# Optimization experiments

Hardware: AMD Instinct MI355X
Metric: run time of the kernel (lower is better)

## Reference

```python
import jax, jax.numpy as jnp
import numpy as np

N_NODES = 4096  # nodes per graph (output1 reshaped to [-1, N_NODES])


def setup_inputs() -> dict:
    key = jax.random.key(0)
    ks = jax.random.split(key, 10)
    total_nodes = 64 * N_NODES          # 64 graphs of 4096 nodes
    n_edges = total_nodes * 8           # avg degree 8 lattice-like graph
    n_hidden = 128
    return {
        "node_features": jax.random.normal(ks[0], (total_nodes, 1), jnp.float32),
        "src": jax.random.randint(ks[1], (n_edges,), 0, total_nodes, jnp.int32),
        "dst": jax.random.randint(ks[2], (n_edges,), 0, total_nodes, jnp.int32),
        "w_self1": jax.random.normal(ks[3], (1, n_hidden), jnp.float32) * 0.5,
        "w_neigh1": jax.random.normal(ks[4], (1, n_hidden), jnp.float32) * 0.5,
        "b1": jnp.zeros((n_hidden,), jnp.float32),
        "w_self2": jax.random.normal(ks[5], (n_hidden, 1), jnp.float32) * (1.0 / np.sqrt(n_hidden)),
        "w_neigh2": jax.random.normal(ks[6], (n_hidden, 1), jnp.float32) * (1.0 / np.sqrt(n_hidden)),
        "b2": jnp.zeros((1,), jnp.float32),
        "w3": jax.random.normal(ks[7], (N_NODES, N_NODES), jnp.float32) * (1.0 / np.sqrt(N_NODES)),
        "b3": jnp.zeros((N_NODES,), jnp.float32),
    }


def _sage_mean(feat, src, dst, w_self, w_neigh, b, num_nodes):
    # gather source-node features along edges, mean-reduce at destination
    agg = jax.ops.segment_sum(feat[src], dst, num_segments=num_nodes)
    deg = jax.ops.segment_sum(jnp.ones((src.shape[0], 1), feat.dtype), dst,
                              num_segments=num_nodes)
    h_neigh = agg / jnp.maximum(deg, 1.0)
    return feat @ w_self + h_neigh @ w_neigh + b


def reference(node_features, src, dst, w_self1, w_neigh1, b1,
              w_self2, w_neigh2, b2, w3, b3):
    n = node_features.shape[0]
    h1 = jnp.tanh(_sage_mean(node_features, src, dst, w_self1, w_neigh1, b1, n))
    out1 = _sage_mean(h1, src, dst, w_self2, w_neigh2, b2, n)
    output1 = out1.reshape(-1, N_NODES)          # [batch, n_nodes]
    h2 = jnp.tanh(output1)
    output2 = h2 @ w3 + b3
    return (output1, output2)
```

## Files before the change

### kernel.cpp

```cpp
#include <hip/hip_runtime.h>


#define NTOT (64 * 4096)
#define NHID 128
#define GK   4096
#define KCH  256
#define KCHUNKS 16
#define GKC  128
#define GKCN 32
#define NBINS 128
#define BSZ   2048
#define BSH   11
#define CAP   17408
#define NSL   4
#define SCB   256

typedef unsigned int u32;

__device__ __forceinline__ float fast_tanh(float x) {
    float ax = fabsf(x);
    float t  = __expf(-2.0f * ax);
    float r  = (1.0f - t) / (1.0f + t);
    return copysignf(r, x);
}


__global__ void __launch_bounds__(1024) scatter_x(const int* __restrict__ src,
                                                  const int* __restrict__ dst,
                                                  int n_edges,
                                                  int* __restrict__ edge_cnt,
                                                  u32* __restrict__ packed) {
    __shared__ int lc[NBINS];
    __shared__ int lbase[NBINS];
    int t = threadIdx.x;
    if (t < NBINS) lc[t] = 0;
    __syncthreads();
    int per = (n_edges + gridDim.x - 1) / gridDim.x;
    int e0 = blockIdx.x * per;
    int e1 = min(e0 + per, n_edges);

    int dreg[8], sreg[8];
#pragma unroll
    for (int i = 0; i < 8; ++i) {
        int e = e0 + t + i * 1024;
        bool ok = e < e1;
        int d = ok ? dst[e] : -1;
        dreg[i] = d;
        sreg[i] = ok ? src[e] : 0;
        if (ok) atomicAdd(&lc[d >> BSH], 1);
    }
    __syncthreads();
    if (t < NBINS) {
        lbase[t] = atomicAdd(&edge_cnt[t], lc[t]);
        lc[t] = 0;
    }
    __syncthreads();
#pragma unroll
    for (int i = 0; i < 8; ++i) {
        int d = dreg[i];
        if (d >= 0) {
            int b = d >> BSH;
            int pos = lbase[b] + atomicAdd(&lc[b], 1);
            if (pos < CAP)
                packed[(size_t)b * CAP + pos] =
                    ((u32)(d & (BSZ - 1)) << 18) | (u32)sreg[i];
        }
    }
}

__global__ void __launch_bounds__(1024) agg1_x(const u32* __restrict__ packed,
                                               const int* __restrict__ edge_cnt,
                                               const float* __restrict__ nf,
                                               float* __restrict__ part1) {
    __shared__ float lsum[BSZ];
    __shared__ float lcnt[BSZ];
    int t = threadIdx.x;
    int b = blockIdx.x, s = blockIdx.y;
    for (int i = t; i < BSZ; i += 1024) { lsum[i] = 0.0f; lcnt[i] = 0.0f; }
    __syncthreads();
    int en  = min(edge_cnt[b], CAP);
    int per = (en + NSL - 1) / NSL;
    int e0  = s * per;
    int e1  = min(e0 + per, en);
    const u32* pk = packed + (size_t)b * CAP;
    for (int e = e0 + t; e < e1; e += 1024) {
        u32 p = pk[e];
        int local = (int)(p >> 18);
        atomicAdd(&lsum[local], nf[p & 0x3FFFFu]);
        atomicAdd(&lcnt[local], 1.0f);
    }
    __syncthreads();
    float* dp = part1 + ((size_t)(b * NSL + s) * 2) * BSZ;
    for (int i = t; i < BSZ; i += 1024) { dp[i] = lsum[i]; dp[BSZ + i] = lcnt[i]; }
}

__global__ void node1_x(const float* __restrict__ nf, const float* __restrict__ part1,
                        const float* __restrict__ w_s1, const float* __restrict__ w_n1,
                        const float* __restrict__ bb1,
                        const float* __restrict__ w_s2, const float* __restrict__ w_n2,
                        float* __restrict__ degf, float* __restrict__ selfp,
                        float* __restrict__ sp) {
    __shared__ float lws1[NHID], lwn1[NHID], lb1[NHID], lws2[NHID], lwn2[NHID];
    int tid = threadIdx.x;
    if (tid < NHID) {
        lws1[tid] = w_s1[tid];
        lwn1[tid] = w_n1[tid];
        lb1[tid]  = bb1[tid];
        lws2[tid] = w_s2[tid];
        lwn2[tid] = w_n2[tid];
    }
    __syncthreads();
    int v = blockIdx.x * blockDim.x + tid;
    int b = v >> BSH, local = v & (BSZ - 1);
    float sum = 0.0f, cf = 0.0f;
#pragma unroll
    for (int s = 0; s < NSL; ++s) {
        const float* dp = part1 + ((size_t)(b * NSL + s) * 2) * BSZ;
        sum += dp[local];
        cf  += dp[BSZ + local];
    }
    float hn = sum / fmaxf(cf, 1.0f);
    float f = nf[v];
    float a = 0.0f, s2 = 0.0f;
#pragma unroll 8
    for (int j = 0; j < NHID; ++j) {
        float t = fast_tanh(fmaf(f, lws1[j], fmaf(hn, lwn1[j], lb1[j])));
        a  = fmaf(t, lws2[j], a);
        s2 = fmaf(t, lwn2[j], s2);
    }
    degf[v]  = cf;
    selfp[v] = a;
    sp[v]    = s2;
}

__global__ void __launch_bounds__(1024) agg2_x(const u32* __restrict__ packed,
                                               const int* __restrict__ edge_cnt,
                                               const float* __restrict__ spv,
                                               float* __restrict__ part2) {
    __shared__ float lsum[BSZ];
    int t = threadIdx.x;
    int b = blockIdx.x, s = blockIdx.y;
    for (int i = t; i < BSZ; i += 1024) lsum[i] = 0.0f;
    __syncthreads();
    int en  = min(edge_cnt[b], CAP);
    int per = (en + NSL - 1) / NSL;
    int e0  = s * per;
    int e1  = min(e0 + per, en);
    const u32* pk = packed + (size_t)b * CAP;
    for (int e = e0 + t; e < e1; e += 1024) {
        u32 p = pk[e];
        atomicAdd(&lsum[p >> 18], spv[p & 0x3FFFFu]);
    }
    __syncthreads();
    float* dp = part2 + (size_t)(b * NSL + s) * BSZ;
    for (int i = t; i < BSZ; i += 1024) dp[i] = lsum[i];
}

__global__ void node2_x(const float* __restrict__ selfp, const float* __restrict__ part2,
                        const float* __restrict__ degf, const float* __restrict__ b2p,
                        const float* __restrict__ b3p,
                        float* __restrict__ out1, float* __restrict__ h2t,
                        float* __restrict__ out2) {
    int v = blockIdx.x * blockDim.x + threadIdx.x;
    int b = v >> BSH, local = v & (BSZ - 1);
    float agg2 = 0.0f;
#pragma unroll
    for (int s = 0; s < NSL; ++s)
        agg2 += part2[(size_t)(b * NSL + s) * BSZ + local];
    float o = selfp[v] + agg2 / fmaxf(degf[v], 1.0f) + b2p[0];
    out1[v] = o;
    int r = v >> 12;
    int k = v & 4095;
    h2t[k * 64 + r] = fast_tanh(o);
    out2[v] = b3p[v & 4095];
}

__global__ void __launch_bounds__(512, 4) gemm_x(const float* __restrict__ h2t,
                                                 const float* __restrict__ w3,
                                                 float* __restrict__ out2) {
    __shared__ float As[GKC * 64 + 64];
    int t    = threadIdx.x;
    int lane = t & 63;
    int wv   = t >> 6;
    int colb = blockIdx.x * 128 + lane * 2;
    int k0   = blockIdx.y * GKC;
    int row0 = __builtin_amdgcn_readfirstlane(wv * 8);

    const float4* gA = (const float4*)(h2t + (size_t)k0 * 64);
    float4* sA = (float4*)As;
#pragma unroll
    for (int i = 0; i < 4; ++i) sA[t + i * 512] = gA[t + i * 512];

    const float* wp  = w3 + (size_t)k0 * GK + colb;
    const float* Asw = As + row0;

    float2 acc[8];
#pragma unroll
    for (int r = 0; r < 8; ++r) { acc[r].x = 0.0f; acc[r].y = 0.0f; }

    float2 bvA[8], bvB[8];
#pragma unroll
    for (int j = 0; j < 8; ++j) bvA[j] = *(const float2*)(wp + (size_t)j * GK);

    __syncthreads();

    float4 a0 = *(const float4*)(Asw);
    float4 a1 = *(const float4*)(Asw + 4);

    for (int kk = 0; kk < GKC; kk += 16) {
#pragma unroll
        for (int j = 0; j < 8; ++j)
            bvB[j] = *(const float2*)(wp + (size_t)(kk + 8 + j) * GK);
#pragma unroll
        for (int j = 0; j < 8; ++j) {
            const float* An = Asw + (kk + j + 1) * 64;
            float4 n0 = *(const float4*)(An);
            float4 n1 = *(const float4*)(An + 4);
            float2 b  = bvA[j];
            acc[0].x = fmaf(a0.x, b.x, acc[0].x); acc[0].y = fmaf(a0.x, b.y, acc[0].y);
            acc[1].x = fmaf(a0.y, b.x, acc[1].x); acc[1].y = fmaf(a0.y, b.y, acc[1].y);
            acc[2].x = fmaf(a0.z, b.x, acc[2].x); acc[2].y = fmaf(a0.z, b.y, acc[2].y);
            acc[3].x = fmaf(a0.w, b.x, acc[3].x); acc[3].y = fmaf(a0.w, b.y, acc[3].y);
            acc[4].x = fmaf(a1.x, b.x, acc[4].x); acc[4].y = fmaf(a1.x, b.y, acc[4].y);
            acc[5].x = fmaf(a1.y, b.x, acc[5].x); acc[5].y = fmaf(a1.y, b.y, acc[5].y);
            acc[6].x = fmaf(a1.z, b.x, acc[6].x); acc[6].y = fmaf(a1.z, b.y, acc[6].y);
            acc[7].x = fmaf(a1.w, b.x, acc[7].x); acc[7].y = fmaf(a1.w, b.y, acc[7].y);
            a0 = n0; a1 = n1;
        }
        if (kk + 16 < GKC) {
#pragma unroll
            for (int j = 0; j < 8; ++j)
                bvA[j] = *(const float2*)(wp + (size_t)(kk + 16 + j) * GK);
        }
#pragma unroll
        for (int j = 0; j < 8; ++j) {
            const float* An = Asw + (kk + 8 + j + 1) * 64;
            float4 n0 = *(const float4*)(An);
            float4 n1 = *(const float4*)(An + 4);
            float2 b  = bvB[j];
            acc[0].x = fmaf(a0.x, b.x, acc[0].x); acc[0].y = fmaf(a0.x, b.y, acc[0].y);
            acc[1].x = fmaf(a0.y, b.x, acc[1].x); acc[1].y = fmaf(a0.y, b.y, acc[1].y);
            acc[2].x = fmaf(a0.z, b.x, acc[2].x); acc[2].y = fmaf(a0.z, b.y, acc[2].y);
            acc[3].x = fmaf(a0.w, b.x, acc[3].x); acc[3].y = fmaf(a0.w, b.y, acc[3].y);
            acc[4].x = fmaf(a1.x, b.x, acc[4].x); acc[4].y = fmaf(a1.x, b.y, acc[4].y);
            acc[5].x = fmaf(a1.y, b.x, acc[5].x); acc[5].y = fmaf(a1.y, b.y, acc[5].y);
            acc[6].x = fmaf(a1.z, b.x, acc[6].x); acc[6].y = fmaf(a1.z, b.y, acc[6].y);
            acc[7].x = fmaf(a1.w, b.x, acc[7].x); acc[7].y = fmaf(a1.w, b.y, acc[7].y);
            a0 = n0; a1 = n1;
        }
    }

    float* Cp = out2 + (size_t)row0 * GK + colb;
#pragma unroll
    for (int r = 0; r < 8; ++r) {
        atomicAdd(Cp + (size_t)r * GK,     acc[r].x);
        atomicAdd(Cp + (size_t)r * GK + 1, acc[r].y);
    }
}


__global__ void edge_pass1_f(const int* __restrict__ src, const int* __restrict__ dst,
                             const float* __restrict__ nf, float* __restrict__ agg,
                             float* __restrict__ deg, int n_edges) {
    int e = blockIdx.x * blockDim.x + threadIdx.x;
    if (e >= n_edges) return;
    int s = src[e], d = dst[e];
    atomicAdd(&agg[d], nf[s]);
    atomicAdd(&deg[d], 1.0f);
}

__global__ void node1_f(const float* __restrict__ nf, float* s0,
                        const float* __restrict__ deg,
                        const float* __restrict__ w_s1, const float* __restrict__ w_n1,
                        const float* __restrict__ bb1,
                        const float* __restrict__ w_s2, const float* __restrict__ w_n2,
                        float* __restrict__ sp) {
    __shared__ float lws1[NHID], lwn1[NHID], lb1[NHID], lws2[NHID], lwn2[NHID];
    int tid = threadIdx.x;
    if (tid < NHID) {
        lws1[tid] = w_s1[tid];
        lwn1[tid] = w_n1[tid];
        lb1[tid]  = bb1[tid];
        lws2[tid] = w_s2[tid];
        lwn2[tid] = w_n2[tid];
    }
    __syncthreads();
    int v = blockIdx.x * blockDim.x + tid;
    float f  = nf[v];
    float hn = s0[v] / fmaxf(deg[v], 1.0f);
    float a = 0.0f, s = 0.0f;
#pragma unroll 8
    for (int j = 0; j < NHID; ++j) {
        float t = fast_tanh(fmaf(f, lws1[j], fmaf(hn, lwn1[j], lb1[j])));
        a = fmaf(t, lws2[j], a);
        s = fmaf(t, lwn2[j], s);
    }
    s0[v] = a;
    sp[v] = s;
}

__global__ void edge_pass2_f(const int* __restrict__ src, const int* __restrict__ dst,
                             const float* __restrict__ sp, float* __restrict__ agg2,
                             int n_edges) {
    int e = blockIdx.x * blockDim.x + threadIdx.x;
    if (e >= n_edges) return;
    atomicAdd(&agg2[dst[e]], sp[src[e]]);
}

__global__ void node2_f(const float* __restrict__ s0, const float* __restrict__ agg2,
                        const float* __restrict__ deg, const float* __restrict__ b2p,
                        const float* __restrict__ b3p,
                        float* __restrict__ out1, float* __restrict__ h2t,
                        float* __restrict__ out2) {
    int v = blockIdx.x * blockDim.x + threadIdx.x;
    float o = s0[v] + agg2[v] / fmaxf(deg[v], 1.0f) + b2p[0];
    out1[v] = o;
    int r = v >> 12;
    int k = v & 4095;
    h2t[k * 64 + r] = fast_tanh(o);
    out2[v] = b3p[v & 4095];
}

__global__ void __launch_bounds__(256) gemm_f(const float* __restrict__ h2t,
                                              const float* __restrict__ w3,
                                              float* __restrict__ out2) {
    int n  = blockIdx.x * 256 + threadIdx.x;
    int k0 = blockIdx.y * KCH;
    float acc[64];
#pragma unroll
    for (int r = 0; r < 64; ++r) acc[r] = 0.0f;
    for (int k = k0; k < k0 + KCH; ++k) {
        float bv = w3[(size_t)k * GK + n];
        const float* Ak = h2t + k * 64;
#pragma unroll
        for (int r = 0; r < 64; ++r) acc[r] = fmaf(Ak[r], bv, acc[r]);
    }
#pragma unroll
    for (int r = 0; r < 64; ++r) atomicAdd(&out2[r * GK + n], acc[r]);
}


extern "C" void kernel_launch(void* const* d_in, const int* in_sizes, int n_in,
                              void* d_out, int out_size, void* d_ws, size_t ws_size,
                              hipStream_t stream) {
    const float* nf  = (const float*)d_in[0];
    const int*   src = (const int*)d_in[1];
    const int*   dst = (const int*)d_in[2];
    const float* ws1 = (const float*)d_in[3];
    const float* wn1 = (const float*)d_in[4];
    const float* b1  = (const float*)d_in[5];
    const float* ws2 = (const float*)d_in[6];
    const float* wn2 = (const float*)d_in[7];
    const float* b2  = (const float*)d_in[8];
    const float* w3  = (const float*)d_in[9];
    const float* b3  = (const float*)d_in[10];
    float* out1 = (float*)d_out;
    float* out2 = (float*)d_out + NTOT;

    int n_edges = in_sizes[1];
    int eb = (n_edges + 255) / 256;

    if (ws_size >= (size_t)20 * 1024 * 1024 && n_edges <= (1 << 21)) {
        char*  base     = (char*)d_ws;
        u32*   packed   = (u32*)base;
        float* part     = (float*)(base + 8912896);
        float* degf     = (float*)(base + 17301504);
        float* selfp    = (float*)(base + 18350080);
        float* spbuf    = (float*)(base + 19398656);
        int*   edge_cnt = (int*)(base + 20447232);
        float* h2t      = spbuf;

        (void)hipMemsetAsync(edge_cnt, 0, NBINS * sizeof(int), stream);
        scatter_x<<<SCB, 1024, 0, stream>>>(src, dst, n_edges, edge_cnt, packed);
        agg1_x<<<dim3(NBINS, NSL), 1024, 0, stream>>>(packed, edge_cnt, nf, part);
        node1_x<<<NTOT / 256, 256, 0, stream>>>(nf, part, ws1, wn1, b1, ws2, wn2,
                                                degf, selfp, spbuf);
        agg2_x<<<dim3(NBINS, NSL), 1024, 0, stream>>>(packed, edge_cnt, spbuf, part);
        node2_x<<<NTOT / 256, 256, 0, stream>>>(selfp, part, degf, b2, b3,
                                                out1, h2t, out2);
        gemm_x<<<dim3(GK / 128, GKCN), 512, 0, stream>>>(h2t, w3, out2);
    } else {
        float* ws = (float*)d_ws;
        float* S0 = ws;
        float* S1 = ws + 1 * NTOT;
        float* S2 = ws + 2 * NTOT;
        float* S3 = ws + 3 * NTOT;

        (void)hipMemsetAsync(S0, 0, (size_t)3 * NTOT * sizeof(float), stream);
        edge_pass1_f<<<eb, 256, 0, stream>>>(src, dst, nf, S0, S1, n_edges);
        node1_f<<<NTOT / 256, 256, 0, stream>>>(nf, S0, S1, ws1, wn1, b1, ws2, wn2, S3);
        edge_pass2_f<<<eb, 256, 0, stream>>>(src, dst, S3, S2, n_edges);
        node2_f<<<NTOT / 256, 256, 0, stream>>>(S0, S2, S1, b2, b3, out1, S3, out2);
        gemm_f<<<dim3(GK / 256, KCHUNKS), 256, 0, stream>>>(S3, w3, out2);
    }
}
```

Baseline: 262.4 us.

## Replace GEMM split-K atomics with per-chunk partial buffers and a reduce kernel

The GEMM split-K count drops from 32 to 16, so each block now covers 256 of K in two staged 128-row shared-memory passes. Each block writes its partial tile with plain float2 stores into a workspace slice instead of doing atomicAdd into out2. A new reduce_x kernel then sums the 16 partials plus the bias, which removes the bias initialisation from node2_x. This trades global atomic contention for 16 MB of extra partial writes and reads plus one more kernel launch, and halves GEMM grid parallelism.

```diff
diff --git a/kernel.cpp b/kernel.cpp
--- a/kernel.cpp
+++ b/kernel.cpp
@@ -7,7 +7,6 @@
 #define KCH  256
 #define KCHUNKS 16
 #define GKC  128
-#define GKCN 32
 #define NBINS 128
 #define BSZ   2048
 #define BSH   11
@@ -158,9 +157,7 @@
 
 __global__ void node2_x(const float* __restrict__ selfp, const float* __restrict__ part2,
                         const float* __restrict__ degf, const float* __restrict__ b2p,
-                        const float* __restrict__ b3p,
-                        float* __restrict__ out1, float* __restrict__ h2t,
-                        float* __restrict__ out2) {
+                        float* __restrict__ out1, float* __restrict__ h2t) {
     int v = blockIdx.x * blockDim.x + threadIdx.x;
     int b = v >> BSH, local = v & (BSZ - 1);
     float agg2 = 0.0f;
@@ -172,90 +169,104 @@
     int r = v >> 12;
     int k = v & 4095;
     h2t[k * 64 + r] = fast_tanh(o);
-    out2[v] = b3p[v & 4095];
 }
 
 __global__ void __launch_bounds__(512, 4) gemm_x(const float* __restrict__ h2t,
                                                  const float* __restrict__ w3,
-                                                 float* __restrict__ out2) {
+                                                 float* __restrict__ Cpart) {
     __shared__ float As[GKC * 64 + 64];
     int t    = threadIdx.x;
     int lane = t & 63;
     int wv   = t >> 6;
     int colb = blockIdx.x * 128 + lane * 2;
-    int k0   = blockIdx.y * GKC;
+    int k0   = blockIdx.y * KCH;
     int row0 = __builtin_amdgcn_readfirstlane(wv * 8);
-
-    const float4* gA = (const float4*)(h2t + (size_t)k0 * 64);
-    float4* sA = (float4*)As;
-#pragma unroll
-    for (int i = 0; i < 4; ++i) sA[t + i * 512] = gA[t + i * 512];
 
     const float* wp  = w3 + (size_t)k0 * GK + colb;
     const float* Asw = As + row0;
+    float4* sA = (float4*)As;
 
     float2 acc[8];
 #pragma unroll
     for (int r = 0; r < 8; ++r) { acc[r].x = 0.0f; acc[r].y = 0.0f; }
 
     float2 bvA[8], bvB[8];
-#pragma unroll
-    for (int j = 0; j < 8; ++j) bvA[j] = *(const float2*)(wp + (size_t)j * GK);
-
-    __syncthreads();
-
-    float4 a0 = *(const float4*)(Asw);
-    float4 a1 = *(const float4*)(Asw + 4);
-
-    for (int kk = 0; kk < GKC; kk += 16) {
+    float4 a0, a1;
+
+#pragma unroll
+    for (int st = 0; st < 2; ++st) {
+        const float* wps = wp + (size_t)(st * GKC) * GK;
+        const float4* gA = (const float4*)(h2t + (size_t)(k0 + st * GKC) * 64);
+        if (st) __syncthreads();
+#pragma unroll
+        for (int i = 0; i < 4; ++i) sA[t + i * 512] = gA[t + i * 512];
 #pragma unroll
         for (int j = 0; j < 8; ++j)
-            bvB[j] = *(const float2*)(wp + (size_t)(kk + 8 + j) * GK);
-#pragma unroll
-        for (int j = 0; j < 8; ++j) {
-            const float* An = Asw + (kk + j + 1) * 64;
-            float4 n0 = *(const float4*)(An);
-            float4 n1 = *(const float4*)(An + 4);
-            float2 b  = bvA[j];
-            acc[0].x = fmaf(a0.x, b.x, acc[0].x); acc[0].y = fmaf(a0.x, b.y, acc[0].y);
-            acc[1].x = fmaf(a0.y, b.x, acc[1].x); acc[1].y = fmaf(a0.y, b.y, acc[1].y);
-            acc[2].x = fmaf(a0.z, b.x, acc[2].x); acc[2].y = fmaf(a0.z, b.y, acc[2].y);
-            acc[3].x = fmaf(a0.w, b.x, acc[3].x); acc[3].y = fmaf(a0.w, b.y, acc[3].y);
-            acc[4].x = fmaf(a1.x, b.x, acc[4].x); acc[4].y = fmaf(a1.x, b.y, acc[4].y);
-            acc[5].x = fmaf(a1.y, b.x, acc[5].x); acc[5].y = fmaf(a1.y, b.y, acc[5].y);
-            acc[6].x = fmaf(a1.z, b.x, acc[6].x); acc[6].y = fmaf(a1.z, b.y, acc[6].y);
-            acc[7].x = fmaf(a1.w, b.x, acc[7].x); acc[7].y = fmaf(a1.w, b.y, acc[7].y);
-            a0 = n0; a1 = n1;
+            bvA[j] = *(const float2*)(wps + (size_t)j * GK);
+        __syncthreads();
+
+        a0 = *(const float4*)(Asw);
+        a1 = *(const float4*)(Asw + 4);
+
+        for (int kk = 0; kk < GKC; kk += 16) {
+#pragma unroll
+            for (int j = 0; j < 8; ++j)
+                bvB[j] = *(const float2*)(wps + (size_t)(kk + 8 + j) * GK);
+#pragma unroll
+            for (int j = 0; j < 8; ++j) {
+                const float* An = Asw + (kk + j + 1) * 64;
+                float4 n0 = *(const float4*)(An);
+                float4 n1 = *(const float4*)(An + 4);
+                float2 b  = bvA[j];
+                acc[0].x = fmaf(a0.x, b.x, acc[0].x); acc[0].y = fmaf(a0.x, b.y, acc[0].y);
+                acc[1].x = fmaf(a0.y, b.x, acc[1].x); acc[1].y = fmaf(a0.y, b.y, acc[1].y);
+                acc[2].x = fmaf(a0.z, b.x, acc[2].x); acc[2].y = fmaf(a0.z, b.y, acc[2].y);
+                acc[3].x = fmaf(a0.w, b.x, acc[3].x); acc[3].y = fmaf(a0.w, b.y, acc[3].y);
+                acc[4].x = fmaf(a1.x, b.x, acc[4].x); acc[4].y = fmaf(a1.x, b.y, acc[4].y);
+                acc[5].x = fmaf(a1.y, b.x, acc[5].x); acc[5].y = fmaf(a1.y, b.y, acc[5].y);
+                acc[6].x = fmaf(a1.z, b.x, acc[6].x); acc[6].y = fmaf(a1.z, b.y, acc[6].y);
+                acc[7].x = fmaf(a1.w, b.x, acc[7].x); acc[7].y = fmaf(a1.w, b.y, acc[7].y);
+                a0 = n0; a1 = n1;
+            }
+            if (kk + 16 < GKC) {
+#pragma unroll
+                for (int j = 0; j < 8; ++j)
+                    bvA[j] = *(const float2*)(wps + (size_t)(kk + 16 + j) * GK);
+            }
+#pragma unroll
+            for (int j = 0; j < 8; ++j) {
+                const float* An = Asw + (kk + 8 + j + 1) * 64;
+                float4 n0 = *(const float4*)(An);
+                float4 n1 = *(const float4*)(An + 4);
+                float2 b  = bvB[j];
+                acc[0].x = fmaf(a0.x, b.x, acc[0].x); acc[0].y = fmaf(a0.x, b.y, acc[0].y);
+                acc[1].x = fmaf(a0.y, b.x, acc[1].x); acc[1].y = fmaf(a0.y, b.y, acc[1].y);
+                acc[2].x = fmaf(a0.z, b.x, acc[2].x); acc[2].y = fmaf(a0.z, b.y, acc[2].y);
+                acc[3].x = fmaf(a0.w, b.x, acc[3].x); acc[3].y = fmaf(a0.w, b.y, acc[3].y);
+                acc[4].x = fmaf(a1.x, b.x, acc[4].x); acc[4].y = fmaf(a1.x, b.y, acc[4].y);
+                acc[5].x = fmaf(a1.y, b.x, acc[5].x); acc[5].y = fmaf(a1.y, b.y, acc[5].y);
+                acc[6].x = fmaf(a1.z, b.x, acc[6].x); acc[6].y = fmaf(a1.z, b.y, acc[6].y);
+                acc[7].x = fmaf(a1.w, b.x, acc[7].x); acc[7].y = fmaf(a1.w, b.y, acc[7].y);
+                a0 = n0; a1 = n1;
+            }
         }
-        if (kk + 16 < GKC) {
-#pragma unroll
-            for (int j = 0; j < 8; ++j)
-                bvA[j] = *(const float2*)(wp + (size_t)(kk + 16 + j) * GK);
-        }
-#pragma unroll
-        for (int j = 0; j < 8; ++j) {
-            const float* An = Asw + (kk + 8 + j + 1) * 64;
-            float4 n0 = *(const float4*)(An);
-            float4 n1 = *(const float4*)(An + 4);
-            float2 b  = bvB[j];
-            acc[0].x = fmaf(a0.x, b.x, acc[0].x); acc[0].y = fmaf(a0.x, b.y, acc[0].y);
-            acc[1].x = fmaf(a0.y, b.x, acc[1].x); acc[1].y = fmaf(a0.y, b.y, acc[1].y);
-            acc[2].x = fmaf(a0.z, b.x, acc[2].x); acc[2].y = fmaf(a0.z, b.y, acc[2].y);
-            acc[3].x = fmaf(a0.w, b.x, acc[3].x); acc[3].y = fmaf(a0.w, b.y, acc[3].y);
-            acc[4].x = fmaf(a1.x, b.x, acc[4].x); acc[4].y = fmaf(a1.x, b.y, acc[4].y);
-            acc[5].x = fmaf(a1.y, b.x, acc[5].x); acc[5].y = fmaf(a1.y, b.y, acc[5].y);
-            acc[6].x = fmaf(a1.z, b.x, acc[6].x); acc[6].y = fmaf(a1.z, b.y, acc[6].y);
-            acc[7].x = fmaf(a1.w, b.x, acc[7].x); acc[7].y = fmaf(a1.w, b.y, acc[7].y);
-            a0 = n0; a1 = n1;
-        }
-    }
-
-    float* Cp = out2 + (size_t)row0 * GK + colb;
-#pragma unroll
-    for (int r = 0; r < 8; ++r) {
-        atomicAdd(Cp + (size_t)r * GK,     acc[r].x);
-        atomicAdd(Cp + (size_t)r * GK + 1, acc[r].y);
-    }
+    }
+
+    float* Cp = Cpart + (size_t)blockIdx.y * NTOT + (size_t)row0 * GK + colb;
+#pragma unroll
+    for (int r = 0; r < 8; ++r) *(float2*)(Cp + (size_t)r * GK) = acc[r];
+}
+
+__global__ void reduce_x(const float4* __restrict__ Cpart, const float4* __restrict__ b3v,
+                         float4* __restrict__ out2) {
+    int v = blockIdx.x * blockDim.x + threadIdx.x;
+    float4 s = b3v[v & 1023];
+#pragma unroll
+    for (int kc = 0; kc < KCHUNKS; ++kc) {
+        float4 c = Cpart[(size_t)kc * (NTOT / 4) + v];
+        s.x += c.x; s.y += c.y; s.z += c.z; s.w += c.w;
+    }
+    out2[v] = s;
 }
 
 
@@ -369,6 +380,7 @@
         float* spbuf    = (float*)(base + 19398656);
         int*   edge_cnt = (int*)(base + 20447232);
         float* h2t      = spbuf;
+        float* Cpart    = (float*)base;
 
         (void)hipMemsetAsync(edge_cnt, 0, NBINS * sizeof(int), stream);
         scatter_x<<<SCB, 1024, 0, stream>>>(src, dst, n_edges, edge_cnt, packed);
@@ -376,9 +388,10 @@
         node1_x<<<NTOT / 256, 256, 0, stream>>>(nf, part, ws1, wn1, b1, ws2, wn2,
                                                 degf, selfp, spbuf);
         agg2_x<<<dim3(NBINS, NSL), 1024, 0, stream>>>(packed, edge_cnt, spbuf, part);
-        node2_x<<<NTOT / 256, 256, 0, stream>>>(selfp, part, degf, b2, b3,
-                                                out1, h2t, out2);
-        gemm_x<<<dim3(GK / 128, GKCN), 512, 0, stream>>>(h2t, w3, out2);
+        node2_x<<<NTOT / 256, 256, 0, stream>>>(selfp, part, degf, b2, out1, h2t);
+        gemm_x<<<dim3(GK / 128, KCHUNKS), 512, 0, stream>>>(h2t, w3, Cpart);
+        reduce_x<<<NTOT / 4 / 256, 256, 0, stream>>>((const float4*)Cpart,
+                                                     (const float4*)b3, (float4*)out2);
     } else {
         float* ws = (float*)d_ws;
         float* S0 = ws;
```

Result: slower. 268.7 us (+2.4%).
